# Kernel optimization log

Hardware: AMD Instinct MI355X
Metric: run time of the kernel (lower is better)

The kernel has to match this reference:

```python
import jax, jax.numpy as jnp
import numpy as np

VOXEL = 64          # voxel_size
MAX_DEPTH = 10.0    # depth_range[1]
SMIN, SMAX = -2.0, 2.0  # spatial_range


def setup_inputs() -> dict:
    key = jax.random.key(0)
    B, H, W = 32, 512, 512
    rgbd = jax.random.uniform(key, (B, 4, H, W), dtype=jnp.float32)
    # scale depth channel to a realistic metric range [0, 8) so that a
    # meaningful fraction of back-projected points falls inside [-2, 2]
    rgbd = rgbd.at[:, 3].multiply(8.0)
    return {"rgbd": rgbd}


def reference(rgbd):
    B, C, H, W = rgbd.shape
    V = VOXEL
    dt = rgbd.dtype

    rgb = jnp.transpose(rgbd[:, :3], (0, 2, 3, 1))   # [B,H,W,3]
    d = rgbd[:, 3]                                   # [B,H,W]

    # intrinsics is None -> default pinhole
    fx = fy = min(H, W) / 2.0
    cx, cy = W / 2.0, H / 2.0

    u = jnp.arange(W, dtype=dt)[None, None, :]       # column index (x)
    v = jnp.arange(H, dtype=dt)[None, :, None]       # row index (y)

    # depth -> pointcloud (per pixel)
    x = (u - cx) * d / fx
    y = (v - cy) * d / fy
    pts = jnp.stack([x, y, d], axis=-1)              # [B,H,W,3]

    depth_valid = (d > 0) & (d < MAX_DEPTH) & jnp.isfinite(d)

    # pointcloud -> voxel coordinates
    coords = jnp.round((pts - SMIN) / (SMAX - SMIN) * (V - 1)).astype(jnp.int32)
    in_range = jnp.all((coords >= 0) & (coords < V), axis=-1)
    mask = depth_valid & in_range                    # [B,H,W]
    coords = jnp.clip(coords, 0, V - 1)

    b_idx = jnp.arange(B, dtype=jnp.int32)[:, None, None]
    lin = ((b_idx * V + coords[..., 0]) * V + coords[..., 1]) * V + coords[..., 2]
    lin = lin.reshape(-1)                            # [B*H*W]
    w = mask.astype(dt).reshape(-1)                  # [B*H*W]

    nseg = B * V * V * V
    count = jax.ops.segment_sum(w, lin, num_segments=nseg)                 # [B*V^3]
    csum = jax.ops.segment_sum(rgb.reshape(-1, 3) * w[:, None], lin,
                               num_segments=nseg)                          # [B*V^3,3]

    occ = (count > 0).astype(dt)                                           # occupancy = 1 where any point lands
    color = jnp.where(count[:, None] > 0,
                      csum / jnp.maximum(count, 1.0)[:, None],
                      jnp.zeros((), dt))                                   # mean color per occupied voxel

    occ = occ.reshape(B, V, V, V)
    color = color.reshape(B, V, V, V, 3).transpose(0, 4, 1, 2, 3)
    return jnp.concatenate([occ[:, None], color], axis=1)  # [B,4,V,V,V]
```

## Files before the change

### kernel.cpp

```cpp
#include <hip/hip_runtime.h>
#include <math.h>


constexpr int V = 64;
constexpr int V3 = V * V * V;
constexpr int Wd = 512, Hd = 512;
constexpr int NPIX = Wd * Hd;
constexpr int NBUCKET = 32 * 64;
constexpr unsigned CAP = 30000;
constexpr float CQ = 32768.0f;
constexpr int PPB = 2048;
constexpr int CHUNKS = NPIX / PPB;

__device__ __forceinline__ bool unproject(int w, int h, float d,
                                          int& ix, int& iy, int& iz) {
    if (!(d > 0.0f) || !(d < 10.0f) || !isfinite(d)) return false;
    const float fx = 256.0f, cx = 256.0f, cy = 256.0f;
    float x = (((float)w - cx) * d) / fx;
    float y = (((float)h - cy) * d) / fx;
    float tx = rintf(((x + 2.0f) * 0.25f) * 63.0f);
    float ty = rintf(((y + 2.0f) * 0.25f) * 63.0f);
    float tz = rintf(((d + 2.0f) * 0.25f) * 63.0f);
    ix = (int)tx; iy = (int)ty; iz = (int)tz;
    return !(ix < 0 || ix >= V || iy < 0 || iy >= V ||
             iz < 0 || iz >= V);
}

__global__ void dtv_cursor_init(unsigned* __restrict__ cursor) {
    int i = blockIdx.x * blockDim.x + threadIdx.x;
    cursor[i] = (unsigned)i * CAP;
}

__global__ void __launch_bounds__(256)
dtv_append4(const float* __restrict__ rgbd,
            unsigned* __restrict__ cursor,
            unsigned long long* __restrict__ entries) {
    int blk = blockIdx.x;
    int b = blk >> 7, chunk = blk & (CHUNKS - 1), t = threadIdx.x;

    __shared__ unsigned lcnt[64];
    __shared__ unsigned lpre[64];
    __shared__ unsigned labs[64];
    __shared__ unsigned long long stage[PPB];
    __shared__ unsigned short bkt[PPB];

    if (t < 64) lcnt[t] = 0;
    __syncthreads();

    const float* bb = rgbd + (size_t)b * 4 * NPIX;
    const float4* r4 = (const float4*)(bb) + chunk * (PPB / 4);
    const float4* g4 = (const float4*)(bb + (size_t)NPIX) + chunk * (PPB / 4);
    const float4* b4 = (const float4*)(bb + (size_t)2 * NPIX) + chunk * (PPB / 4);
    const float4* d4 = (const float4*)(bb + (size_t)3 * NPIX) + chunk * (PPB / 4);
    int pbase = chunk * PPB;

    float4 dv[2], rv[2], gv[2], bv[2];
#pragma unroll
    for (int i = 0; i < 2; ++i) dv[i] = d4[t + i * 256];
#pragma unroll
    for (int i = 0; i < 2; ++i) {
        rv[i] = r4[t + i * 256];
        gv[i] = g4[t + i * 256];
        bv[i] = b4[t + i * 256];
    }

    unsigned meta[8];
#pragma unroll
    for (int i = 0; i < 2; ++i) {
        int p0 = pbase + 4 * (t + i * 256);
#pragma unroll
        for (int j = 0; j < 4; ++j) {
            float d = (j == 0) ? dv[i].x : (j == 1) ? dv[i].y
                    : (j == 2) ? dv[i].z : dv[i].w;
            int pix = p0 + j;
            int h = pix >> 9, w = pix & (Wd - 1);
            int ix, iy, iz;
            if (unproject(w, h, d, ix, iy, iz)) {
                unsigned off = atomicAdd(&lcnt[ix], 1u);
                meta[i * 4 + j] = ((unsigned)ix << 24) | ((unsigned)iy << 18) |
                                  ((unsigned)iz << 12) | off;
            } else {
                meta[i * 4 + j] = 0xFFFFFFFFu;
            }
        }
    }
    __syncthreads();

    if (t < 64) {
        unsigned c = lcnt[t];
        unsigned s = c;
#pragma unroll
        for (int off = 1; off < 64; off <<= 1) {
            unsigned v = __shfl_up(s, off, 64);
            if (t >= off) s += v;
        }
        lpre[t] = s - c;
        labs[t] = c ? atomicAdd(&cursor[b * 64 + t], c) : 0u;
    }
    __syncthreads();

#pragma unroll
    for (int i = 0; i < 2; ++i) {
#pragma unroll
        for (int j = 0; j < 4; ++j) {
            unsigned m = meta[i * 4 + j];
            if (m == 0xFFFFFFFFu) continue;
            unsigned ix = m >> 24, iy = (m >> 18) & 63u, iz = (m >> 12) & 63u;
            unsigned off = m & 0xFFFu;
            float r  = (j == 0) ? rv[i].x : (j == 1) ? rv[i].y
                     : (j == 2) ? rv[i].z : rv[i].w;
            float g  = (j == 0) ? gv[i].x : (j == 1) ? gv[i].y
                     : (j == 2) ? gv[i].z : gv[i].w;
            float bl = (j == 0) ? bv[i].x : (j == 1) ? bv[i].y
                     : (j == 2) ? bv[i].z : bv[i].w;
            unsigned long long r16 = (unsigned long long)(unsigned)rintf(r  * CQ);
            unsigned long long g16 = (unsigned long long)(unsigned)rintf(g  * CQ);
            unsigned long long b16 = (unsigned long long)(unsigned)rintf(bl * CQ);
            unsigned slot = lpre[ix] + off;
            stage[slot] = ((unsigned long long)iy << 54) |
                          ((unsigned long long)iz << 48) |
                          (r16 << 32) | (g16 << 16) | b16;
            bkt[slot] = (unsigned short)ix;
        }
    }
    __syncthreads();

    unsigned total = lpre[63] + lcnt[63];
    for (unsigned e = t; e < total; e += 256) {
        unsigned ix = bkt[e];
        unsigned pos = labs[ix] + (e - lpre[ix]);
        unsigned kk = (unsigned)(b * 64) + ix;
        if (pos < (kk + 1) * CAP)
            entries[(size_t)pos] = stage[e];
    }
}

__global__ void __launch_bounds__(512)
dtv_reduce3(const ulonglong2* __restrict__ entries2,
            const unsigned* __restrict__ cursor,
            float* __restrict__ out) {
    int kk = blockIdx.x;
    int b = kk >> 6, ix = kk & 63, t = threadIdx.x;

    __shared__ unsigned long long ldsA[4096];
    __shared__ unsigned long long ldsB[4096];
    ulonglong2* zA = (ulonglong2*)ldsA;
    ulonglong2* zB = (ulonglong2*)ldsB;
#pragma unroll
    for (int i = 0; i < 4; ++i) {
        zA[t * 4 + i] = ulonglong2{0ULL, 0ULL};
        zB[t * 4 + i] = ulonglong2{0ULL, 0ULL};
    }
    __syncthreads();

    auto accum = [&](unsigned long long p) {
        unsigned iy = (unsigned)(p >> 54) & 63u;
        unsigned iz = (unsigned)(p >> 48) & 63u;
        unsigned v = iy * 64u + iz;
        atomicAdd(&ldsA[v], (1ULL << 32) | ((p >> 32) & 0xFFFFULL));
        atomicAdd(&ldsB[v], (((p >> 16) & 0xFFFFULL) << 32) | (p & 0xFFFFULL));
    };

    unsigned basew = (unsigned)kk * CAP;
    unsigned cnt = cursor[kk] - basew;
    if (cnt > CAP) cnt = CAP;
    unsigned npair = cnt >> 1;
    size_t base2 = (size_t)kk * (CAP / 2);
    for (unsigned j = t; j < npair; j += 512) {
        ulonglong2 e2 = entries2[base2 + j];
        accum(e2.x);
        accum(e2.y);
    }
    if ((cnt & 1u) && t == 0) {
        const unsigned long long* e1 = (const unsigned long long*)entries2;
        accum(e1[(size_t)basew + cnt - 1]);
    }
    __syncthreads();

    float* p0 = out + (size_t)b * 4 * V3 + (size_t)ix * 4096;
#pragma unroll
    for (int i = 0; i < 2; ++i) {
        int v0 = (i * 512 + t) * 4;
        float4 o0, o1, o2, o3;
#pragma unroll
        for (int j = 0; j < 4; ++j) {
            unsigned long long A = ldsA[v0 + j], Bw = ldsB[v0 + j];
            unsigned c = (unsigned)(A >> 32);
            float occ = 0.0f, r = 0.0f, g = 0.0f, bl = 0.0f;
            if (c) {
                float inv = 1.0f / (CQ * (float)c);
                occ = 1.0f;
                r  = (float)(unsigned)(A  & 0xFFFFFFFFULL) * inv;
                g  = (float)(unsigned)(Bw >> 32)            * inv;
                bl = (float)(unsigned)(Bw & 0xFFFFFFFFULL)  * inv;
            }
            (&o0.x)[j] = occ; (&o1.x)[j] = r; (&o2.x)[j] = g; (&o3.x)[j] = bl;
        }
        int q = v0 >> 2;
        ((float4*)(p0))[q]                    = o0;
        ((float4*)(p0 + (size_t)V3))[q]       = o1;
        ((float4*)(p0 + (size_t)2 * V3))[q]   = o2;
        ((float4*)(p0 + (size_t)3 * V3))[q]   = o3;
    }
}

__global__ void dtv_scatter_f32(const float* __restrict__ rgbd,
                                float* __restrict__ acc) {
    int idx = blockIdx.x * blockDim.x + threadIdx.x;
    int b   = idx >> 18;
    int pix = idx & (NPIX - 1);
    int h   = pix >> 9;
    int w   = pix & (Wd - 1);
    const float* base = rgbd + (size_t)b * 4 * NPIX;
    float d = base[(size_t)3 * NPIX + pix];
    int ix, iy, iz;
    if (!unproject(w, h, d, ix, iy, iz)) return;
    float r  = base[pix];
    float g  = base[(size_t)NPIX + pix];
    float bl = base[(size_t)2 * NPIX + pix];
    float* ob = acc + (size_t)b * 4 * V3;
    int vlin = (ix * V + iy) * V + iz;
    atomicAdd(ob + vlin, 1.0f);
    atomicAdd(ob + (size_t)V3 + vlin, r);
    atomicAdd(ob + (size_t)2 * V3 + vlin, g);
    atomicAdd(ob + (size_t)3 * V3 + vlin, bl);
}

__global__ void dtv_finalize_f32(float* __restrict__ out) {
    int idx = blockIdx.x * blockDim.x + threadIdx.x;
    int b    = idx >> 18;
    int vlin = idx & (V3 - 1);
    float* p = out + (size_t)b * 4 * V3;
    float c  = p[vlin];
    float r  = p[(size_t)V3 + vlin];
    float g  = p[(size_t)2 * V3 + vlin];
    float bl = p[(size_t)3 * V3 + vlin];
    bool occ = (c > 0.0f);
    p[vlin]                  = occ ? 1.0f : 0.0f;
    p[(size_t)V3 + vlin]     = occ ? (r / c)  : 0.0f;
    p[(size_t)2 * V3 + vlin] = occ ? (g / c)  : 0.0f;
    p[(size_t)3 * V3 + vlin] = occ ? (bl / c) : 0.0f;
}

extern "C" void kernel_launch(void* const* d_in, const int* in_sizes, int n_in,
                              void* d_out, int out_size, void* d_ws, size_t ws_size,
                              hipStream_t stream) {
    const float* rgbd = (const float*)d_in[0];
    float* out = (float*)d_out;
    const int B = in_sizes[0] / (4 * NPIX);

    size_t need = 8192 + (size_t)NBUCKET * CAP * sizeof(unsigned long long);

    if (B == 32 && ws_size >= need) {
        unsigned* cursor = (unsigned*)d_ws;
        unsigned long long* entries =
            (unsigned long long*)((char*)d_ws + 8192);
        dtv_cursor_init<<<NBUCKET / 256, 256, 0, stream>>>(cursor);
        dtv_append4    <<<B * CHUNKS, 256, 0, stream>>>(rgbd, cursor, entries);
        dtv_reduce3    <<<NBUCKET, 512, 0, stream>>>((const ulonglong2*)entries,
                                                     cursor, out);
    } else {
        hipMemsetAsync(d_out, 0, (size_t)out_size * sizeof(float), stream);
        int total_pix = B * NPIX;
        int total_vox = B * V3;
        dtv_scatter_f32 <<<(total_pix + 255) / 256, 256, 0, stream>>>(rgbd, out);
        dtv_finalize_f32<<<(total_vox + 255) / 256, 256, 0, stream>>>(out);
    }
}
```

Before: 248.5 us.

## Split voxel reduction into four iy-quadrant blocks per bucket with prefetch

```diff
diff --git a/kernel.cpp b/kernel.cpp
--- a/kernel.cpp
+++ b/kernel.cpp
@@ -135,41 +135,51 @@
     }
 }
 
-__global__ void __launch_bounds__(512)
-dtv_reduce3(const ulonglong2* __restrict__ entries2,
+__global__ void __launch_bounds__(256)
+dtv_reduce4(const ulonglong2* __restrict__ entries2,
             const unsigned* __restrict__ cursor,
             float* __restrict__ out) {
-    int kk = blockIdx.x;
+    int bq = blockIdx.x;
+    int kk = bq >> 2;
+    unsigned quad = (unsigned)(bq & 3);
     int b = kk >> 6, ix = kk & 63, t = threadIdx.x;
 
-    __shared__ unsigned long long ldsA[4096];
-    __shared__ unsigned long long ldsB[4096];
-    ulonglong2* zA = (ulonglong2*)ldsA;
-    ulonglong2* zB = (ulonglong2*)ldsB;
-#pragma unroll
-    for (int i = 0; i < 4; ++i) {
-        zA[t * 4 + i] = ulonglong2{0ULL, 0ULL};
-        zB[t * 4 + i] = ulonglong2{0ULL, 0ULL};
-    }
-    __syncthreads();
-
-    auto accum = [&](unsigned long long p) {
-        unsigned iy = (unsigned)(p >> 54) & 63u;
-        unsigned iz = (unsigned)(p >> 48) & 63u;
-        unsigned v = iy * 64u + iz;
-        atomicAdd(&ldsA[v], (1ULL << 32) | ((p >> 32) & 0xFFFFULL));
-        atomicAdd(&ldsB[v], (((p >> 16) & 0xFFFFULL) << 32) | (p & 0xFFFFULL));
-    };
+    __shared__ unsigned long long ldsA[1024];
+    __shared__ unsigned long long ldsB[1024];
 
     unsigned basew = (unsigned)kk * CAP;
     unsigned cnt = cursor[kk] - basew;
     if (cnt > CAP) cnt = CAP;
     unsigned npair = cnt >> 1;
     size_t base2 = (size_t)kk * (CAP / 2);
-    for (unsigned j = t; j < npair; j += 512) {
-        ulonglong2 e2 = entries2[base2 + j];
-        accum(e2.x);
-        accum(e2.y);
+
+    ulonglong2 e2;
+    if (t < (int)npair) e2 = entries2[base2 + t];
+
+    ulonglong2* zA = (ulonglong2*)ldsA;
+    ulonglong2* zB = (ulonglong2*)ldsB;
+#pragma unroll
+    for (int i = 0; i < 2; ++i) {
+        zA[t + i * 256] = ulonglong2{0ULL, 0ULL};
+        zB[t + i * 256] = ulonglong2{0ULL, 0ULL};
+    }
+    __syncthreads();
+
+    auto accum = [&](unsigned long long p) {
+        if (((unsigned)(p >> 58) & 3u) != quad) return;
+        unsigned iy4 = (unsigned)(p >> 54) & 15u;
+        unsigned iz  = (unsigned)(p >> 48) & 63u;
+        unsigned v = iy4 * 64u + iz;
+        atomicAdd(&ldsA[v], (1ULL << 32) | ((p >> 32) & 0xFFFFULL));
+        atomicAdd(&ldsB[v], (((p >> 16) & 0xFFFFULL) << 32) | (p & 0xFFFFULL));
+    };
+
+    for (unsigned j = t; j < npair; j += 256) {
+        ulonglong2 cur = e2;
+        unsigned jn = j + 256;
+        if (jn < npair) e2 = entries2[base2 + jn];
+        accum(cur.x);
+        accum(cur.y);
     }
     if ((cnt & 1u) && t == 0) {
         const unsigned long long* e1 = (const unsigned long long*)entries2;
@@ -177,31 +187,27 @@
     }
     __syncthreads();
 
-    float* p0 = out + (size_t)b * 4 * V3 + (size_t)ix * 4096;
-#pragma unroll
-    for (int i = 0; i < 2; ++i) {
-        int v0 = (i * 512 + t) * 4;
-        float4 o0, o1, o2, o3;
-#pragma unroll
-        for (int j = 0; j < 4; ++j) {
-            unsigned long long A = ldsA[v0 + j], Bw = ldsB[v0 + j];
-            unsigned c = (unsigned)(A >> 32);
-            float occ = 0.0f, r = 0.0f, g = 0.0f, bl = 0.0f;
-            if (c) {
-                float inv = 1.0f / (CQ * (float)c);
-                occ = 1.0f;
-                r  = (float)(unsigned)(A  & 0xFFFFFFFFULL) * inv;
-                g  = (float)(unsigned)(Bw >> 32)            * inv;
-                bl = (float)(unsigned)(Bw & 0xFFFFFFFFULL)  * inv;
-            }
-            (&o0.x)[j] = occ; (&o1.x)[j] = r; (&o2.x)[j] = g; (&o3.x)[j] = bl;
-        }
-        int q = v0 >> 2;
-        ((float4*)(p0))[q]                    = o0;
-        ((float4*)(p0 + (size_t)V3))[q]       = o1;
-        ((float4*)(p0 + (size_t)2 * V3))[q]   = o2;
-        ((float4*)(p0 + (size_t)3 * V3))[q]   = o3;
-    }
+    float* p0 = out + (size_t)b * 4 * V3 + (size_t)ix * 4096 + quad * 1024;
+    int v0 = t * 4;
+    float4 o0, o1, o2, o3;
+#pragma unroll
+    for (int j = 0; j < 4; ++j) {
+        unsigned long long A = ldsA[v0 + j], Bw = ldsB[v0 + j];
+        unsigned c = (unsigned)(A >> 32);
+        float occ = 0.0f, r = 0.0f, g = 0.0f, bl = 0.0f;
+        if (c) {
+            float inv = 1.0f / (CQ * (float)c);
+            occ = 1.0f;
+            r  = (float)(unsigned)(A  & 0xFFFFFFFFULL) * inv;
+            g  = (float)(unsigned)(Bw >> 32)            * inv;
+            bl = (float)(unsigned)(Bw & 0xFFFFFFFFULL)  * inv;
+        }
+        (&o0.x)[j] = occ; (&o1.x)[j] = r; (&o2.x)[j] = g; (&o3.x)[j] = bl;
+    }
+    ((float4*)(p0))[t]                  = o0;
+    ((float4*)(p0 + (size_t)V3))[t]     = o1;
+    ((float4*)(p0 + (size_t)2 * V3))[t] = o2;
+    ((float4*)(p0 + (size_t)3 * V3))[t] = o3;
 }
 
 __global__ void dtv_scatter_f32(const float* __restrict__ rgbd,
@@ -257,8 +263,8 @@
             (unsigned long long*)((char*)d_ws + 8192);
         dtv_cursor_init<<<NBUCKET / 256, 256, 0, stream>>>(cursor);
         dtv_append4    <<<B * CHUNKS, 256, 0, stream>>>(rgbd, cursor, entries);
-        dtv_reduce3    <<<NBUCKET, 512, 0, stream>>>((const ulonglong2*)entries,
-                                                     cursor, out);
+        dtv_reduce4    <<<NBUCKET * 4, 256, 0, stream>>>((const ulonglong2*)entries,
+                                                         cursor, out);
     } else {
         hipMemsetAsync(d_out, 0, (size_t)out_size * sizeof(float), stream);
         int total_pix = B * NPIX;
```

New measurement: 246.4 us. No clear change (-0.8%).
